# Kernel tuning notes

Hardware: AMD Instinct MI355X
Metric: run time of the kernel (lower is better)

## Reference

```python
import jax, jax.numpy as jnp
import numpy as np

T, DIM, HID = 8192, 1024, 4096

def setup_inputs() -> dict:
    key = jax.random.key(0)
    k1, k2, k3 = jax.random.split(key, 3)
    x = jax.random.normal(k1, (T, DIM), dtype=jnp.float32)
    # torch Linear weight layout: [out_features, in_features]
    W_fc = jax.random.normal(k2, (HID, DIM), dtype=jnp.float32) * 0.02
    W_proj = jax.random.normal(k3, (DIM, HID), dtype=jnp.float32) * 0.02
    return {"x": x, "W_fc": W_fc, "W_proj": W_proj}

def reference(x, W_fc, W_proj):
    # fc: x @ W_fc^T  -> relu -> square -> proj: @ W_proj^T
    h = jnp.einsum('td,hd->th', x, W_fc)      # [T, HID]
    h = jnp.square(jax.nn.relu(h))            # relu(h)^2 (relu^2 activation)
    return jnp.einsum('th,dh->td', h, W_proj) # [T, DIM]
```

## Files before the change

kernel.cpp:

```cpp
#include <hip/hip_runtime.h>
#include <stdint.h>


#define BM 128
#define BN 128
#define BK 32

typedef __attribute__((ext_vector_type(8))) short bf16x8;
typedef __attribute__((ext_vector_type(4))) float f32x4;

typedef const __attribute__((address_space(1))) unsigned int* gas_u32p;
typedef __attribute__((address_space(3))) unsigned int* las_u32p;

__device__ __forceinline__ void load16_to_lds(const void* gptr, void* lptr) {
    __builtin_amdgcn_global_load_lds((gas_u32p)gptr, (las_u32p)lptr, 16, 0, 0);
}

__device__ __forceinline__ unsigned short f2bf(float f) {
    unsigned int u = __float_as_uint(f);
    u += 0x7FFFu + ((u >> 16) & 1u);
    return (unsigned short)(u >> 16);
}

__global__ void cvt_f32_bf16(const float4* __restrict__ src,
                             ushort4* __restrict__ dst, int n4)
{
    int i = blockIdx.x * blockDim.x + threadIdx.x;
    int stride = gridDim.x * blockDim.x;
    for (; i < n4; i += stride) {
        float4 v = src[i];
        ushort4 o;
        o.x = f2bf(v.x); o.y = f2bf(v.y); o.z = f2bf(v.z); o.w = f2bf(v.w);
        dst[i] = o;
    }
}

template<bool RELU2, bool OUT_BF16>
__global__ __launch_bounds__(256, 3)
void gemm_bt(const unsigned short* __restrict__ A,
             const unsigned short* __restrict__ B,
             void* __restrict__ Cv, int M, int N, int K)
{
    __shared__ unsigned short sA[BM * BK];
    __shared__ unsigned short sB[BN * BK];

    const int tid  = threadIdx.x;
    const int lane = tid & 63;
    const int wave = tid >> 6;
    const int wm   = (wave >> 1) * 64;
    const int wn   = (wave & 1) * 64;
    const int quad = lane >> 4;
    const int m16  = lane & 15;

    const long bm0 = (long)blockIdx.y * BM;
    const long bn0 = (long)blockIdx.x * BN;

    const int srow = tid >> 2;
    const int scol = (tid & 3) * 8;

    const unsigned short* gA = A + (bm0 + srow) * (long)K + scol;
    const unsigned short* gB = B + (bn0 + srow) * (long)K + scol;
    char* lA = (char*)sA + tid * 16;
    char* lB = (char*)sB + tid * 16;

    f32x4 acc[4][4];
    #pragma unroll
    for (int i = 0; i < 4; i++)
        #pragma unroll
        for (int j = 0; j < 4; j++)
            acc[i][j] = (f32x4)0.0f;

    for (int k0 = 0; k0 < K; k0 += BK) {
        load16_to_lds(gA + k0,                lA);
        load16_to_lds(gA + 64 * (long)K + k0, lA + 4096);
        load16_to_lds(gB + k0,                lB);
        load16_to_lds(gB + 64 * (long)K + k0, lB + 4096);
        __syncthreads();

        bf16x8 af[4], bfr[4];
        #pragma unroll
        for (int i = 0; i < 4; i++)
            af[i]  = *(const bf16x8*)&sA[(wm + i * 16 + m16) * BK + quad * 8];
        #pragma unroll
        for (int j = 0; j < 4; j++)
            bfr[j] = *(const bf16x8*)&sB[(wn + j * 16 + m16) * BK + quad * 8];

        #pragma unroll
        for (int i = 0; i < 4; i++)
            #pragma unroll
            for (int j = 0; j < 4; j++)
                acc[i][j] = __builtin_amdgcn_mfma_f32_16x16x32_bf16(
                    af[i], bfr[j], acc[i][j], 0, 0, 0);

        __syncthreads();
    }

    #pragma unroll
    for (int i = 0; i < 4; i++) {
        #pragma unroll
        for (int j = 0; j < 4; j++) {
            #pragma unroll
            for (int r = 0; r < 4; r++) {
                float v = acc[i][j][r];
                if (RELU2) v = (v > 0.0f) ? v * v : 0.0f;
                const long row = bm0 + wm + i * 16 + quad * 4 + r;
                const long col = bn0 + wn + j * 16 + m16;
                if (OUT_BF16)
                    ((unsigned short*)Cv)[row * (long)N + col] = f2bf(v);
                else
                    ((float*)Cv)[row * (long)N + col] = v;
            }
        }
    }
}

extern "C" void kernel_launch(void* const* d_in, const int* in_sizes, int n_in,
                              void* d_out, int out_size, void* d_ws, size_t ws_size,
                              hipStream_t stream) {
    (void)in_sizes; (void)n_in; (void)out_size; (void)ws_size;

    const int T = 8192, DIM = 1024, HID = 4096;

    const float* x     = (const float*)d_in[0];
    const float* W_fc  = (const float*)d_in[1];
    const float* W_prj = (const float*)d_in[2];
    float* out = (float*)d_out;

    char* ws = (char*)d_ws;
    unsigned short* h   = (unsigned short*)ws;
    unsigned short* xb  = (unsigned short*)(ws + (64l << 20));
    unsigned short* wfb = (unsigned short*)(ws + (80l << 20));
    unsigned short* wpb = (unsigned short*)(ws + (88l << 20));

    const int nx = T * DIM / 4, nw1 = HID * DIM / 4, nw2 = DIM * HID / 4;
    cvt_f32_bf16<<<1024, 256, 0, stream>>>((const float4*)x,     (ushort4*)xb,  nx);
    cvt_f32_bf16<<<1024, 256, 0, stream>>>((const float4*)W_fc,  (ushort4*)wfb, nw1);
    cvt_f32_bf16<<<1024, 256, 0, stream>>>((const float4*)W_prj, (ushort4*)wpb, nw2);

    gemm_bt<true, true><<<dim3(HID / BN, T / BM), dim3(256), 0, stream>>>(
        xb, wfb, h, T, HID, DIM);

    gemm_bt<false, false><<<dim3(DIM / BN, T / BM), dim3(256), 0, stream>>>(
        h, wpb, out, T, DIM, HID);
}
```

Before: 276.6 us.

## Register-prefetch GEMM tiles, swizzle block order for XCD locality, fuse conversions

Three separate changes. The direct global-to-LDS loads are replaced by register prefetching, so the next K-tile is loaded into registers while the current tile is computed and then stored to LDS. Workgroup ids are remapped so blocks on the same XCD share row or column tiles, aiming for better L2 reuse. The three fp32-to-bf16 conversion launches are merged into one kernel. Prefetching raises register pressure under launch_bounds(256,3), and it still uses a single LDS buffer with two barriers per step.

```diff
diff --git a/kernel.cpp b/kernel.cpp
--- a/kernel.cpp
+++ b/kernel.cpp
@@ -9,33 +9,32 @@
 typedef __attribute__((ext_vector_type(8))) short bf16x8;
 typedef __attribute__((ext_vector_type(4))) float f32x4;
 
-typedef const __attribute__((address_space(1))) unsigned int* gas_u32p;
-typedef __attribute__((address_space(3))) unsigned int* las_u32p;
-
-__device__ __forceinline__ void load16_to_lds(const void* gptr, void* lptr) {
-    __builtin_amdgcn_global_load_lds((gas_u32p)gptr, (las_u32p)lptr, 16, 0, 0);
-}
-
 __device__ __forceinline__ unsigned short f2bf(float f) {
     unsigned int u = __float_as_uint(f);
     u += 0x7FFFu + ((u >> 16) & 1u);
     return (unsigned short)(u >> 16);
 }
 
-__global__ void cvt_f32_bf16(const float4* __restrict__ src,
-                             ushort4* __restrict__ dst, int n4)
+__global__ void cvt3_f32_bf16(const float4* __restrict__ s0, ushort4* __restrict__ d0, int n0,
+                              const float4* __restrict__ s1, ushort4* __restrict__ d1, int n1,
+                              const float4* __restrict__ s2, ushort4* __restrict__ d2, int n2)
 {
     int i = blockIdx.x * blockDim.x + threadIdx.x;
-    int stride = gridDim.x * blockDim.x;
-    for (; i < n4; i += stride) {
-        float4 v = src[i];
+    const int stride = gridDim.x * blockDim.x;
+    const int ntot = n0 + n1 + n2;
+    for (; i < ntot; i += stride) {
+        const float4* s; ushort4* d; int j = i;
+        if (j < n0)             { s = s0; d = d0; }
+        else if ((j -= n0) < n1){ s = s1; d = d1; }
+        else                    { j -= n1; s = s2; d = d2; }
+        float4 v = s[j];
         ushort4 o;
         o.x = f2bf(v.x); o.y = f2bf(v.y); o.z = f2bf(v.z); o.w = f2bf(v.w);
-        dst[i] = o;
+        d[j] = o;
     }
 }
 
-template<bool RELU2, bool OUT_BF16>
+template<bool RELU2, bool OUT_BF16, int SWIZ>
 __global__ __launch_bounds__(256, 3)
 void gemm_bt(const unsigned short* __restrict__ A,
              const unsigned short* __restrict__ B,
@@ -52,14 +51,27 @@
     const int quad = lane >> 4;
     const int m16  = lane & 15;
 
-    const long bm0 = (long)blockIdx.y * BM;
-    const long bn0 = (long)blockIdx.x * BN;
+    const int lbid = blockIdx.y * gridDim.x + blockIdx.x;
+    int bx, by;
+    if (SWIZ == 1) {
+        bx = lbid & 7;
+        by = lbid >> 3;
+    } else {
+        const int xcd = lbid & 7;
+        const int t   = lbid >> 3;
+        by = xcd * 8 + (t & 7);
+        bx = t >> 3;
+    }
+
+    const long bm0 = (long)by * BM;
+    const long bn0 = (long)bx * BN;
 
     const int srow = tid >> 2;
     const int scol = (tid & 3) * 8;
 
-    const unsigned short* gA = A + (bm0 + srow) * (long)K + scol;
-    const unsigned short* gB = B + (bn0 + srow) * (long)K + scol;
+    const unsigned short* pA = A + (bm0 + srow) * (long)K + scol;
+    const unsigned short* pB = B + (bn0 + srow) * (long)K + scol;
+    const long strideA = 64 * (long)K;
     char* lA = (char*)sA + tid * 16;
     char* lB = (char*)sB + tid * 16;
 
@@ -70,12 +82,25 @@
         for (int j = 0; j < 4; j++)
             acc[i][j] = (f32x4)0.0f;
 
+    uint4 ra0 = *(const uint4*)(pA);
+    uint4 ra1 = *(const uint4*)(pA + strideA);
+    uint4 rb0 = *(const uint4*)(pB);
+    uint4 rb1 = *(const uint4*)(pB + strideA);
+
     for (int k0 = 0; k0 < K; k0 += BK) {
-        load16_to_lds(gA + k0,                lA);
-        load16_to_lds(gA + 64 * (long)K + k0, lA + 4096);
-        load16_to_lds(gB + k0,                lB);
-        load16_to_lds(gB + 64 * (long)K + k0, lB + 4096);
+        *(uint4*)lA          = ra0;
+        *(uint4*)(lA + 4096) = ra1;
+        *(uint4*)lB          = rb0;
+        *(uint4*)(lB + 4096) = rb1;
         __syncthreads();
+
+        if (k0 + BK < K) {
+            pA += BK; pB += BK;
+            ra0 = *(const uint4*)(pA);
+            ra1 = *(const uint4*)(pA + strideA);
+            rb0 = *(const uint4*)(pB);
+            rb1 = *(const uint4*)(pB + strideA);
+        }
 
         bf16x8 af[4], bfr[4];
         #pragma unroll
@@ -132,14 +157,14 @@
     unsigned short* wfb = (unsigned short*)(ws + (80l << 20));
     unsigned short* wpb = (unsigned short*)(ws + (88l << 20));
 
-    const int nx = T * DIM / 4, nw1 = HID * DIM / 4, nw2 = DIM * HID / 4;
-    cvt_f32_bf16<<<1024, 256, 0, stream>>>((const float4*)x,     (ushort4*)xb,  nx);
-    cvt_f32_bf16<<<1024, 256, 0, stream>>>((const float4*)W_fc,  (ushort4*)wfb, nw1);
-    cvt_f32_bf16<<<1024, 256, 0, stream>>>((const float4*)W_prj, (ushort4*)wpb, nw2);
+    cvt3_f32_bf16<<<2048, 256, 0, stream>>>(
+        (const float4*)x,     (ushort4*)xb,  T * DIM / 4,
+        (const float4*)W_fc,  (ushort4*)wfb, HID * DIM / 4,
+        (const float4*)W_prj, (ushort4*)wpb, DIM * HID / 4);
 
-    gemm_bt<true, true><<<dim3(HID / BN, T / BM), dim3(256), 0, stream>>>(
+    gemm_bt<true, true, 0><<<dim3(HID / BN, T / BM), dim3(256), 0, stream>>>(
         xb, wfb, h, T, HID, DIM);
 
-    gemm_bt<false, false><<<dim3(DIM / BN, T / BM), dim3(256), 0, stream>>>(
+    gemm_bt<false, false, 1><<<dim3(DIM / BN, T / BM), dim3(256), 0, stream>>>(
         h, wpb, out, T, DIM, HID);
 }
```

New measurement: 276.3 us. Within noise of the previous version (-0.1%).
